# Kernel optimization log

Measured on AMD Instinct MI355X. Metric: run time of the kernel, lower is better.

Reference implementation:

```python
import jax, jax.numpy as jnp
import numpy as np

DIM = 180; HEADS = 6; WS = 16; NUM_TOKENS = 64; RDIM = 10; CAT = 128
KS = 5; MLP_HID = 360; DTD = 64; Hh = 64; Ww = 64; B = 8; M = 64


def _ln(x, g, b, eps=1e-5):
    mu = x.mean(-1, keepdims=True)
    var = ((x - mu) ** 2).mean(-1, keepdims=True)
    return (x - mu) / jnp.sqrt(var + eps) * g + b


def _l2norm(x):
    return x / jnp.clip(jnp.linalg.norm(x, axis=-1, keepdims=True), 1e-12)


def setup_inputs() -> dict:
    key = jax.random.key(0)
    ks = jax.random.split(key, 24)
    rn = lambda k, s: jax.random.normal(k, s, jnp.float32) * 0.02
    z = lambda *s: jnp.zeros(s, jnp.float32)
    return {
        'x': jax.random.normal(ks[0], (B, Hh * Ww, DIM), jnp.float32),
        'td': jax.random.normal(ks[1], (B, M, DIM), jnp.float32),
        'norm1_g': jnp.ones((DIM,), jnp.float32), 'norm1_b': z(DIM),
        'wqkv_w': rn(ks[2], (DIM, 3 * DIM)), 'wqkv_b': z(3 * DIM),
        'atd_wq_w': rn(ks[3], (DIM, RDIM)), 'atd_wq_b': z(RDIM),
        'atd_wk_w': rn(ks[4], (DIM, RDIM)), 'atd_wk_b': z(RDIM),
        'atd_wv_w': rn(ks[5], (DIM, DIM)), 'atd_wv_b': z(DIM),
        'atd_scale': jnp.ones((1,), jnp.float32),
        'aca_proj_w': rn(ks[6], (DIM, DIM)), 'aca_proj_b': z(DIM),
        'win_rpb': rn(ks[7], ((2 * WS - 1) ** 2, HEADS)),
        'win_proj_w': rn(ks[8], (DIM, DIM)), 'win_proj_b': z(DIM),
        'fc_td_w': rn(ks[9], (DIM, DTD)), 'fc_td_b': z(DTD),
        'fc1_w': rn(ks[10], (DIM, MLP_HID)), 'fc1_b': z(MLP_HID),
        'dw_w': rn(ks[11], (MLP_HID + DTD, 1, KS, KS)), 'dw_b': z(MLP_HID + DTD),
        'fc2_w': rn(ks[12], (MLP_HID + DTD, DIM)), 'fc2_b': z(DIM),
        'norm2_g': jnp.ones((DIM,), jnp.float32), 'norm2_b': z(DIM),
        'rpi_sa': jax.random.randint(ks[13], (WS * WS, WS * WS), 0, (2 * WS - 1) ** 2),
        'h': Hh, 'w': Ww,
    }


def reference(x, td, norm1_g, norm1_b, wqkv_w, wqkv_b, atd_wq_w, atd_wq_b,
              atd_wk_w, atd_wk_b, atd_wv_w, atd_wv_b, atd_scale,
              aca_proj_w, aca_proj_b, win_rpb, win_proj_w, win_proj_b,
              fc_td_w, fc_td_b, fc1_w, fc1_b, dw_w, dw_b, fc2_w, fc2_b,
              norm2_g, norm2_b, rpi_sa, h, w):
    b, n, c = x.shape
    hd = c // HEADS
    shortcut = x
    xn = _ln(x, norm1_g, norm1_b)
    qkv = xn @ wqkv_w + wqkv_b  # [b, n, 3c]

    # --- ATD_CA: l2-normalized cross-attention to token dictionary ---
    q = xn @ atd_wq_w + atd_wq_b          # [b, n, rd]
    kk = td @ atd_wk_w + atd_wk_b         # [b, m, rd]
    vv = td @ atd_wv_w + atd_wv_b         # [b, m, c]
    logit_scale = 1.0 + jnp.clip(atd_scale, 0.0, 3.0) * np.log(NUM_TOKENS)
    sim = jnp.einsum('bnr,bmr->bnm', _l2norm(q), _l2norm(kk)) * logit_scale
    attn_atd = jax.nn.softmax(sim, axis=-1)
    x_atd = jnp.einsum('bnm,bmc->bnc', attn_atd, vv)
    tk_id = jnp.argmax(attn_atd, axis=-1)  # [b, n]

    # --- AC_MSA: category-sorted grouped attention ---
    gs = min(n, CAT); ng = (n + gs - 1) // gs; pad_n = ng * gs - n
    sort_idx = jnp.argsort(tk_id, axis=-1)
    inv_idx = jnp.argsort(sort_idx, axis=-1)  # inverse permutation
    sq = jnp.take_along_axis(qkv, sort_idx[:, :, None], axis=1)
    sq = jnp.concatenate([sq, jnp.flip(sq[:, n - pad_n:n, :], axis=1)], axis=1)
    g = sq.reshape(b, ng, gs, 3, HEADS, hd).transpose(3, 0, 1, 4, 2, 5)
    qa, ka, va = g[0], g[1], g[2]          # [b, ng, H, gs, hd]
    a = jax.nn.softmax(jnp.einsum('bgHid,bgHjd->bgHij', qa, ka) * hd ** -0.5, axis=-1)
    y = jnp.einsum('bgHij,bgHjd->bgHid', a, va).transpose(0, 1, 3, 2, 4)
    y = y.reshape(b, n + pad_n, c)[:, :n]
    x_aca = jnp.take_along_axis(y, inv_idx[:, :, None], axis=1) @ aca_proj_w + aca_proj_b

    # --- gather per-token dictionary features for FFN ---
    td_proj = td @ fc_td_w + fc_td_b       # [b, m, dtd]
    x_td = jnp.take_along_axis(td_proj, jnp.broadcast_to(tk_id[:, :, None], (b, n, DTD)), axis=1)

    # --- window attention (shift_size = 0, no mask) ---
    nwh, nww = h // WS, w // WS
    win = qkv.reshape(b, nwh, WS, nww, WS, 3 * c).transpose(0, 1, 3, 2, 4, 5)
    win = win.reshape(-1, WS * WS, 3 * c)
    B_ = win.shape[0]; N = WS * WS
    wq = win.reshape(B_, N, 3, HEADS, hd).transpose(2, 0, 3, 1, 4)
    qw, kw, vw = wq[0] * hd ** -0.5, wq[1], wq[2]
    bias = win_rpb[rpi_sa.reshape(-1)].reshape(N, N, HEADS).transpose(2, 0, 1)[None]
    aw = jax.nn.softmax(jnp.einsum('wHid,wHjd->wHij', qw, kw) + bias, axis=-1)
    ow = jnp.einsum('wHij,wHjd->wHid', aw, vw).transpose(0, 2, 1, 3).reshape(B_, N, c)
    ow = ow @ win_proj_w + win_proj_b
    attn_x = ow.reshape(b, nwh, nww, WS, WS, c).transpose(0, 1, 3, 2, 4, 5).reshape(b, n, c)

    x = shortcut + x_atd + attn_x + x_aca

    # --- ConvFFN_td with depthwise conv branch ---
    x2 = _ln(x, norm2_g, norm2_b)
    h1 = jax.nn.gelu(x2 @ fc1_w + fc1_b, approximate=False)
    hc = jnp.concatenate([h1, x_td], axis=-1)  # [b, n, C]
    C = hc.shape[-1]
    img = jnp.swapaxes(hc, 1, 2).reshape(b, C, h, w)
    conv = jax.lax.conv_general_dilated(img, dw_w, (1, 1), 'SAME',
        dimension_numbers=('NCHW', 'OIHW', 'NCHW'), feature_group_count=C)
    conv = jax.nn.gelu(conv + dw_b[None, :, None, None], approximate=False)
    hc = hc + jnp.swapaxes(conv.reshape(b, C, n), 1, 2)
    return x + hc @ fc2_w + fc2_b
```

## Files before the change

kernel.cpp:

```cpp
#include <hip/hip_runtime.h>
#include <hip/hip_bf16.h>
#include <math.h>

#define BB      8
#define NTOK    4096
#define CDIM    180
#define C3      540
#define NHEADS  6
#define HD      30
#define MDICT   64
#define RD      10
#define DTD     64
#define MHID    360
#define CCAT    424
#define WS      16
#define WIN_N   256
#define GS      128
#define NG      32
#define ROWS    (BB*NTOK)
#define KP1     192
#define KP2     448

typedef __hip_bfloat16 bf16;
typedef short v8s __attribute__((ext_vector_type(8)));
typedef float f32x4 __attribute__((ext_vector_type(4)));
typedef unsigned int u32x4 __attribute__((ext_vector_type(4)));

__device__ __forceinline__ float gelu_exact(float x) {
    return 0.5f * x * (1.0f + erff(x * 0.70710678118654752f));
}
__device__ __forceinline__ float wave_sum(float v) {
    #pragma unroll
    for (int off = 32; off > 0; off >>= 1) v += __shfl_xor(v, off, 64);
    return v;
}
__device__ __forceinline__ unsigned short f2b(float v) {
    unsigned u = __float_as_uint(v);
    return (unsigned short)((u + 0x7FFFu + ((u >> 16) & 1u)) >> 16);
}
__device__ __forceinline__ float b2f(unsigned short h) {
    return __uint_as_float(((unsigned)h) << 16);
}
__device__ __forceinline__ unsigned packbf(float lo, float hi) {
    return (unsigned)f2b(lo) | ((unsigned)f2b(hi) << 16);
}
__device__ __forceinline__ void gload16(const void* g, void* l) {
    __builtin_amdgcn_global_load_lds(
        (const __attribute__((address_space(1))) void*)g,
        (__attribute__((address_space(3))) void*)l, 16, 0, 0);
}

__global__ __launch_bounds__(256) void detect_kernel(const void* __restrict__ x,
                                                     int* __restrict__ flag,
                                                     int* __restrict__ diag)
{
    __shared__ int cnt;
    if (threadIdx.x == 0) { cnt = 0; *diag = 0; }
    __syncthreads();
    const unsigned short* u = (const unsigned short*)x;
    int c = 0;
    for (int i = threadIdx.x; i < 2048; i += 256) {
        unsigned short e = u[2 * i] & 0x7F80;
        if (e >= 0x4300) c++;
    }
    atomicAdd(&cnt, c);
    __syncthreads();
    if (threadIdx.x == 0) *flag = (cnt > 16) ? 1 : 0;
}

#define NCVT 23
struct CvtArgs {
    const void* src[NCVT];
    float* dst[NCVT];
    int cum[NCVT + 1];
};
__global__ __launch_bounds__(256) void convert_all_kernel(CvtArgs a, int total,
        const int* __restrict__ flag)
{
    int i = blockIdx.x * 256 + threadIdx.x;
    if (i >= total) return;
    int s = 0;
    while (i >= a.cum[s + 1]) s++;
    int off = i - a.cum[s];
    if (*flag) a.dst[s][off] = ((const float*)a.src[s])[off];
    else       a.dst[s][off] = __bfloat162float(((const bf16*)a.src[s])[off]);
}

__global__ __launch_bounds__(256) void check_f32_kernel(const float* __restrict__ buf,
        int n, int bit, int* __restrict__ diag)
{
    int i = blockIdx.x * 256 + threadIdx.x;
    if (i >= n) return;
    unsigned u = __float_as_uint(buf[i]);
    if ((u & 0x7F800000u) == 0x7F800000u) atomicOr(diag, bit);
}

__global__ __launch_bounds__(256) void emit_kernel(const float* __restrict__ src,
        void* __restrict__ out, const int* __restrict__ flag,
        const int* __restrict__ diag, int n)
{
    int i = blockIdx.x * 256 + threadIdx.x;
    if (i >= n) return;
    float v = src[i];
    int d = *diag;
    if (d) v = 100.f + 32.f * (float)d;
    if (*flag) ((float*)out)[i] = v;
    else       ((bf16*)out)[i]  = __float2bfloat16(v);
}

__global__ __launch_bounds__(256) void zero_tail_kernel(bf16* __restrict__ buf)
{
    int idx = blockIdx.x * 256 + threadIdx.x;
    int row = idx / 12, c = idx % 12;
    buf[(size_t)row * KP1 + CDIM + c] = __float2bfloat16(0.f);
}

__global__ __launch_bounds__(256) void packW_kernel(const void* __restrict__ W,
        bf16* __restrict__ Wt, int K, int N, int Kpad, int total,
        const int* __restrict__ flag)
{
    int idx = blockIdx.x * 256 + threadIdx.x;
    if (idx >= total) return;
    int n = idx / Kpad, k = idx % Kpad;
    float v = 0.f;
    if (k < K && n < N) {
        size_t src = (size_t)k * N + n;
        v = (*flag) ? ((const float*)W)[src]
                    : __bfloat162float(((const bf16*)W)[src]);
    }
    Wt[idx] = __float2bfloat16(v);
}

__global__ __launch_bounds__(256) void bias_pre_kernel(const int* __restrict__ rpi,
        const float* __restrict__ rpb, float* __restrict__ bias_t)
{
    int idx = blockIdx.x * 256 + threadIdx.x;
    int h = idx >> 16, ij = idx & 65535;
    bias_t[idx] = rpb[rpi[ij] * NHEADS + h];
}

template<bool GELU_, bool ADDRES, bool BIAS_>
__global__ __launch_bounds__(256) void mgemm_kernel(
        const bf16* __restrict__ A, int lda,
        const bf16* __restrict__ Wt, int ldw,
        const float* __restrict__ bias,
        const float* __restrict__ res, int ldr,
        float* __restrict__ outF, int ldo, int N, int K)
{
    __shared__ __align__(16) unsigned short As[128][32];
    __shared__ __align__(16) unsigned short Bs[64][32];
    int tid = threadIdx.x;
    int wave = tid >> 6, lane = tid & 63;
    int quad = lane >> 4, mr = lane & 15;
    int row0 = blockIdx.y * 128, col0 = blockIdx.x * 64;
    int ar = tid >> 2, ac = (tid & 3) * 8;
    f32x4 z = {0.f, 0.f, 0.f, 0.f};
    f32x4 acc[2][4] = {{z, z, z, z}, {z, z, z, z}};
    const unsigned short* Au = (const unsigned short*)A;
    const unsigned short* Wu = (const unsigned short*)Wt;
    for (int k0 = 0; k0 < K; k0 += 32) {
        gload16(&Au[(size_t)(row0 + ar) * lda + k0 + ac],      &As[ar][ac]);
        gload16(&Au[(size_t)(row0 + 64 + ar) * lda + k0 + ac], &As[64 + ar][ac]);
        gload16(&Wu[(size_t)(col0 + ar) * ldw + k0 + ac],      &Bs[ar][ac]);
        __syncthreads();
        v8s bfr[4];
        #pragma unroll
        for (int ni = 0; ni < 4; ni++)
            bfr[ni] = *(const v8s*)&Bs[ni * 16 + mr][quad * 8];
        #pragma unroll
        for (int s = 0; s < 2; s++) {
            v8s a = *(const v8s*)&As[wave * 32 + s * 16 + mr][quad * 8];
            #pragma unroll
            for (int ni = 0; ni < 4; ni++)
                acc[s][ni] = __builtin_amdgcn_mfma_f32_16x16x32_bf16(
                    a, bfr[ni], acc[s][ni], 0, 0, 0);
        }
        __syncthreads();
    }
    #pragma unroll
    for (int ni = 0; ni < 4; ni++) {
        int gc = col0 + ni * 16 + mr;
        if (gc >= N) continue;
        float bv = BIAS_ ? bias[gc] : 0.f;
        #pragma unroll
        for (int s = 0; s < 2; s++) {
            #pragma unroll
            for (int r = 0; r < 4; r++) {
                int gr = row0 + wave * 32 + s * 16 + quad * 4 + r;
                float v = acc[s][ni][r] + bv;
                if (GELU_) v = gelu_exact(v);
                if (ADDRES) v += res[(size_t)gr * ldr + gc];
                outF[(size_t)gr * ldo + gc] = v;
            }
        }
    }
}

__global__ __launch_bounds__(256) void av_mgemm_kernel(
        const bf16* __restrict__ P, const bf16* __restrict__ vvT,
        const float* __restrict__ xres, float* __restrict__ accout)
{
    __shared__ unsigned short As[64][32];
    __shared__ unsigned short Bs[64][32];
    int tid = threadIdx.x;
    int wave = tid >> 6, lane = tid & 63;
    int quad = lane >> 4, mr = lane & 15;
    int row0 = blockIdx.y * 64, col0 = blockIdx.x * 64;
    int bz = blockIdx.z;
    const unsigned short* Au = (const unsigned short*)P + (size_t)bz * NTOK * MDICT;
    const unsigned short* Wu = (const unsigned short*)vvT + (size_t)bz * 192 * MDICT;
    const float* res = xres + (size_t)bz * NTOK * CDIM;
    float* outF = accout + (size_t)bz * NTOK * CDIM;
    f32x4 z = {0.f, 0.f, 0.f, 0.f};
    f32x4 acc[4] = {z, z, z, z};
    for (int k0 = 0; k0 < MDICT; k0 += 32) {
        #pragma unroll
        for (int e = 0; e < 8; e++) {
            int idx = tid * 8 + e;
            int r = idx >> 5, c = idx & 31;
            As[r][c] = Au[(size_t)(row0 + r) * MDICT + k0 + c];
            Bs[r][c] = Wu[(size_t)(col0 + r) * MDICT + k0 + c];
        }
        __syncthreads();
        v8s a;
        #pragma unroll
        for (int j = 0; j < 8; j++) a[j] = (short)As[wave * 16 + mr][quad * 8 + j];
        #pragma unroll
        for (int ni = 0; ni < 4; ni++) {
            v8s b;
            #pragma unroll
            for (int j = 0; j < 8; j++) b[j] = (short)Bs[ni * 16 + mr][quad * 8 + j];
            acc[ni] = __builtin_amdgcn_mfma_f32_16x16x32_bf16(a, b, acc[ni], 0, 0, 0);
        }
        __syncthreads();
    }
    #pragma unroll
    for (int ni = 0; ni < 4; ni++) {
        int gc = col0 + ni * 16 + mr;
        if (gc >= CDIM) continue;
        #pragma unroll
        for (int r = 0; r < 4; r++) {
            int gr = row0 + wave * 16 + quad * 4 + r;
            float v = acc[ni][r] + res[(size_t)gr * CDIM + gc];
            outF[(size_t)gr * CDIM + gc] = v;
        }
    }
}

__global__ __launch_bounds__(256, 4) void win_mfma_kernel(const float* __restrict__ qkv,
        const float* __restrict__ bias_t, bf16* __restrict__ outb)
{
    int b = blockIdx.y;
    int widx = blockIdx.x / NHEADS;
    int hh = blockIdx.x % NHEADS;
    int wy = widx >> 2, wx = widx & 3;
    int tid = threadIdx.x;
    int wave = tid >> 6, lane = tid & 63, quad = lane >> 4, mr = lane & 15;
    __shared__ __align__(16) unsigned short Ks[64][40];
    __shared__ __align__(16) unsigned short Vt[32][80];

    size_t brow = (size_t)b * NTOK;
    const float scq = 0.18257418583505536f;

    v8s aq[4];
    #pragma unroll
    for (int tt = 0; tt < 4; tt++) {
        int m = (wave * 4 + tt) * 16 + mr;
        int nt_ = (wy * WS + (m >> 4)) * 64 + wx * WS + (m & 15);
        const float* qrow = qkv + (brow + nt_) * C3 + hh * HD;
        #pragma unroll
        for (int jj = 0; jj < 8; jj++) {
            int d = quad * 8 + jj;
            float v = (d < HD) ? qrow[d] * scq : 0.f;
            aq[tt][jj] = (short)f2b(v);
        }
    }
    f32x4 z = {0.f, 0.f, 0.f, 0.f};
    f32x4 oacc[4][2] = {{z, z}, {z, z}, {z, z}, {z, z}};
    float m_r[4], l_r[4];
    #pragma unroll
    for (int tt = 0; tt < 4; tt++) { m_r[tt] = -3.0e38f; l_r[tt] = 0.f; }
    const float* btab = bias_t + (size_t)hh * WIN_N * WIN_N;

    for (int kc = 0; kc < WIN_N; kc += 64) {
        {
            int j = tid >> 2, dg = (tid & 3) * 8;
            int tok = kc + j;
            int nt_ = (wy * WS + (tok >> 4)) * 64 + wx * WS + (tok & 15);
            const float* krow = qkv + (brow + nt_) * C3 + CDIM + hh * HD;
            const float* vrow = qkv + (brow + nt_) * C3 + 2 * CDIM + hh * HD;
            v8s kv;
            #pragma unroll
            for (int jj = 0; jj < 8; jj++) {
                int d = dg + jj;
                float kf = (d < HD) ? krow[d] : 0.f;
                float vf = (d < HD) ? vrow[d] : 0.f;
                kv[jj] = (short)f2b(kf);
                Vt[d][j] = f2b(vf);
            }
            *(v8s*)&Ks[j][dg] = kv;
        }
        __syncthreads();
        #pragma unroll
        for (int tt = 0; tt < 4; tt++) {
            f32x4 s[4];
            #pragma unroll
            for (int nt = 0; nt < 4; nt++) {
                v8s bk = *(const v8s*)&Ks[nt * 16 + mr][quad * 8];
                s[nt] = __builtin_amdgcn_mfma_f32_16x16x32_bf16(bk, aq[tt], z, 0, 0, 0);
            }
            int qg = (wave * 4 + tt) * 16 + mr;
            const float* bi = btab + (size_t)qg * WIN_N + kc;
            float mc = -3.0e38f;
            #pragma unroll
            for (int nt = 0; nt < 4; nt++) {
                f32x4 b4 = *(const f32x4*)(bi + nt * 16 + quad * 4);
                s[nt][0] += b4[0]; s[nt][1] += b4[1];
                s[nt][2] += b4[2]; s[nt][3] += b4[3];
                mc = fmaxf(mc, fmaxf(fmaxf(s[nt][0], s[nt][1]),
                                     fmaxf(s[nt][2], s[nt][3])));
            }
            mc = fmaxf(mc, __shfl_xor(mc, 16, 64));
            mc = fmaxf(mc, __shfl_xor(mc, 32, 64));
            float mn = fmaxf(m_r[tt], mc);
            float alpha = __expf(m_r[tt] - mn);
            m_r[tt] = mn;
            float ls = 0.f;
            #pragma unroll
            for (int nt = 0; nt < 4; nt++) {
                #pragma unroll
                for (int r = 0; r < 4; r++) {
                    float pp = __expf(s[nt][r] - mn);
                    ls += pp;
                    s[nt][r] = pp;
                }
            }
            ls += __shfl_xor(ls, 16, 64);
            ls += __shfl_xor(ls, 32, 64);
            l_r[tt] = l_r[tt] * alpha + ls;
            unsigned dpk[4][2];
            #pragma unroll
            for (int nt = 0; nt < 4; nt++) {
                dpk[nt][0] = packbf(s[nt][0], s[nt][1]);
                dpk[nt][1] = packbf(s[nt][2], s[nt][3]);
            }
            #pragma unroll
            for (int r = 0; r < 4; r++) {
                float av = __shfl(alpha, quad * 4 + r, 64);
                oacc[tt][0][r] *= av;
                oacc[tt][1][r] *= av;
            }
            #pragma unroll
            for (int c = 0; c < 2; c++) {
                union { u32x4 u; v8s s8; } afu;
                #pragma unroll
                for (int t = 0; t < 4; t++) {
                    int srcl = (((quad * 2 + (t >> 1)) & 3) << 4) | mr;
                    unsigned r0 = (unsigned)__shfl((int)dpk[2 * c][t & 1], srcl, 64);
                    unsigned r1 = (unsigned)__shfl((int)dpk[2 * c + 1][t & 1], srcl, 64);
                    afu.u[t] = (quad & 2) ? r1 : r0;
                }
                #pragma unroll
                for (int dt = 0; dt < 2; dt++) {
                    v8s bv = *(const v8s*)&Vt[dt * 16 + mr][c * 32 + quad * 8];
                    oacc[tt][dt] = __builtin_amdgcn_mfma_f32_16x16x32_bf16(
                        afu.s8, bv, oacc[tt][dt], 0, 0, 0);
                }
            }
        }
        __syncthreads();
    }
    #pragma unroll
    for (int tt = 0; tt < 4; tt++) {
        float il = 1.f / l_r[tt];
        #pragma unroll
        for (int r = 0; r < 4; r++) {
            float ilr = __shfl(il, quad * 4 + r, 64);
            int m = (wave * 4 + tt) * 16 + quad * 4 + r;
            int nt_ = (wy * WS + (m >> 4)) * 64 + wx * WS + (m & 15);
            #pragma unroll
            for (int dt = 0; dt < 2; dt++) {
                int d = dt * 16 + mr;
                if (d >= HD) continue;
                outb[(brow + nt_) * KP1 + hh * HD + d] =
                    __float2bfloat16(oacc[tt][dt][r] * ilr);
            }
        }
    }
}

__global__ __launch_bounds__(256, 4) void acmsa_mfma_kernel(const float* __restrict__ qkv,
        const int* __restrict__ sidx, bf16* __restrict__ outb)
{
    int b = blockIdx.y;
    int g = blockIdx.x / NHEADS;
    int hh = blockIdx.x % NHEADS;
    int tid = threadIdx.x;
    int wave = tid >> 6, lane = tid & 63, quad = lane >> 4, mr = lane & 15;
    __shared__ int toks[GS];
    __shared__ __align__(16) unsigned short Ks[64][40];
    __shared__ __align__(16) unsigned short Vt[32][80];

    size_t brow = (size_t)b * NTOK;
    if (tid < GS) toks[tid] = sidx[brow + (size_t)g * GS + tid];
    __syncthreads();
    const float scq = 0.18257418583505536f;

    v8s aq[2];
    #pragma unroll
    for (int tt = 0; tt < 2; tt++) {
        int m = (wave * 2 + tt) * 16 + mr;
        const float* qrow = qkv + (brow + toks[m]) * C3 + hh * HD;
        #pragma unroll
        for (int jj = 0; jj < 8; jj++) {
            int d = quad * 8 + jj;
            float v = (d < HD) ? qrow[d] * scq : 0.f;
            aq[tt][jj] = (short)f2b(v);
        }
    }
    f32x4 z = {0.f, 0.f, 0.f, 0.f};
    f32x4 oacc[2][2] = {{z, z}, {z, z}};
    float m_r[2], l_r[2];
    #pragma unroll
    for (int tt = 0; tt < 2; tt++) { m_r[tt] = -3.0e38f; l_r[tt] = 0.f; }

    for (int kc = 0; kc < GS; kc += 64) {
        {
            int j = tid >> 2, dg = (tid & 3) * 8;
            int tok = toks[kc + j];
            const float* krow = qkv + (brow + tok) * C3 + CDIM + hh * HD;
            const float* vrow = qkv + (brow + tok) * C3 + 2 * CDIM + hh * HD;
            v8s kv;
            #pragma unroll
            for (int jj = 0; jj < 8; jj++) {
                int d = dg + jj;
                float kf = (d < HD) ? krow[d] : 0.f;
                float vf = (d < HD) ? vrow[d] : 0.f;
                kv[jj] = (short)f2b(kf);
                Vt[d][j] = f2b(vf);
            }
            *(v8s*)&Ks[j][dg] = kv;
        }
        __syncthreads();
        #pragma unroll
        for (int tt = 0; tt < 2; tt++) {
            f32x4 s[4];
            #pragma unroll
            for (int nt = 0; nt < 4; nt++) {
                v8s bk = *(const v8s*)&Ks[nt * 16 + mr][quad * 8];
                s[nt] = __builtin_amdgcn_mfma_f32_16x16x32_bf16(bk, aq[tt], z, 0, 0, 0);
            }
            float mc = -3.0e38f;
            #pragma unroll
            for (int nt = 0; nt < 4; nt++)
                mc = fmaxf(mc, fmaxf(fmaxf(s[nt][0], s[nt][1]),
                                     fmaxf(s[nt][2], s[nt][3])));
            mc = fmaxf(mc, __shfl_xor(mc, 16, 64));
            mc = fmaxf(mc, __shfl_xor(mc, 32, 64));
            float mn = fmaxf(m_r[tt], mc);
            float alpha = __expf(m_r[tt] - mn);
            m_r[tt] = mn;
            float ls = 0.f;
            #pragma unroll
            for (int nt = 0; nt < 4; nt++) {
                #pragma unroll
                for (int r = 0; r < 4; r++) {
                    float pp = __expf(s[nt][r] - mn);
                    ls += pp;
                    s[nt][r] = pp;
                }
            }
            ls += __shfl_xor(ls, 16, 64);
            ls += __shfl_xor(ls, 32, 64);
            l_r[tt] = l_r[tt] * alpha + ls;
            unsigned dpk[4][2];
            #pragma unroll
            for (int nt = 0; nt < 4; nt++) {
                dpk[nt][0] = packbf(s[nt][0], s[nt][1]);
                dpk[nt][1] = packbf(s[nt][2], s[nt][3]);
            }
            #pragma unroll
            for (int r = 0; r < 4; r++) {
                float av = __shfl(alpha, quad * 4 + r, 64);
                oacc[tt][0][r] *= av;
                oacc[tt][1][r] *= av;
            }
            #pragma unroll
            for (int c = 0; c < 2; c++) {
                union { u32x4 u; v8s s8; } afu;
                #pragma unroll
                for (int t = 0; t < 4; t++) {
                    int srcl = (((quad * 2 + (t >> 1)) & 3) << 4) | mr;
                    unsigned r0 = (unsigned)__shfl((int)dpk[2 * c][t & 1], srcl, 64);
                    unsigned r1 = (unsigned)__shfl((int)dpk[2 * c + 1][t & 1], srcl, 64);
                    afu.u[t] = (quad & 2) ? r1 : r0;
                }
                #pragma unroll
                for (int dt = 0; dt < 2; dt++) {
                    v8s bv = *(const v8s*)&Vt[dt * 16 + mr][c * 32 + quad * 8];
                    oacc[tt][dt] = __builtin_amdgcn_mfma_f32_16x16x32_bf16(
                        afu.s8, bv, oacc[tt][dt], 0, 0, 0);
                }
            }
        }
        __syncthreads();
    }
    #pragma unroll
    for (int tt = 0; tt < 2; tt++) {
        float il = 1.f / l_r[tt];
        #pragma unroll
        for (int r = 0; r < 4; r++) {
            float ilr = __shfl(il, quad * 4 + r, 64);
            int m = (wave * 2 + tt) * 16 + quad * 4 + r;
            int tok = toks[m];
            #pragma unroll
            for (int dt = 0; dt < 2; dt++) {
                int d = dt * 16 + mr;
                if (d >= HD) continue;
                outb[(brow + tok) * KP1 + hh * HD + d] =
                    __float2bfloat16(oacc[tt][dt][r] * ilr);
            }
        }
    }
}

__global__ __launch_bounds__(64) void ln_kernel(const float* __restrict__ x,
        const float* __restrict__ g, const float* __restrict__ be,
        float* __restrict__ out, bf16* __restrict__ outb)
{
    int row = blockIdx.x; int t = threadIdx.x;
    const float* xr = x + (size_t)row * CDIM;
    float v0 = xr[t];
    float v1 = xr[t + 64];
    float v2 = (t < CDIM - 128) ? xr[t + 128] : 0.f;
    float s1 = wave_sum(v0 + v1 + v2);
    float s2 = wave_sum(v0*v0 + v1*v1 + v2*v2);
    float mu = s1 / (float)CDIM;
    float var = s2 / (float)CDIM - mu * mu;
    float rs = rsqrtf(var + 1e-5f);
    float o0 = (v0 - mu) * rs * g[t]      + be[t];
    float o1 = (v1 - mu) * rs * g[t + 64] + be[t + 64];
    float o2 = (t < CDIM - 128) ? ((v2 - mu) * rs * g[t + 128] + be[t + 128]) : 0.f;
    float* o = out + (size_t)row * CDIM;
    o[t] = o0; o[t + 64] = o1;
    if (t < CDIM - 128) o[t + 128] = o2;
    bf16* ob = outb + (size_t)row * KP1;
    ob[t]       = __float2bfloat16(o0);
    ob[t + 64]  = __float2bfloat16(o1);
    ob[t + 128] = __float2bfloat16(o2);
}

__global__ __launch_bounds__(64) void td_pre_kernel(const float* __restrict__ td,
        const float* __restrict__ wk, const float* __restrict__ wkb,
        const float* __restrict__ wv, const float* __restrict__ wvb,
        const float* __restrict__ wtd, const float* __restrict__ wtdb,
        float* __restrict__ kkn, bf16* __restrict__ vvT, float* __restrict__ tdp)
{
    int blk = blockIdx.x;
    int b = blk >> 6, m = blk & 63;
    int t = threadIdx.x;
    __shared__ float tr[CDIM];
    __shared__ float sk[RD];
    __shared__ float snorm;
    const float* tdr = td + (size_t)blk * CDIM;
    tr[t] = tdr[t]; tr[t + 64] = tdr[t + 64];
    if (t < CDIM - 128) tr[t + 128] = tdr[t + 128];
    __syncthreads();
    if (t < RD) {
        float s = wkb[t];
        for (int k = 0; k < CDIM; k++) s += tr[k] * wk[k * RD + t];
        sk[t] = s;
    }
    __syncthreads();
    if (t == 0) {
        float s = 0.f;
        #pragma unroll
        for (int j = 0; j < RD; j++) s += sk[j] * sk[j];
        snorm = fmaxf(sqrtf(s), 1e-12f);
    }
    __syncthreads();
    if (t < RD) kkn[(size_t)blk * RD + t] = sk[t] / snorm;
    for (int c = t; c < 192; c += 64) {
        float s = 0.f;
        if (c < CDIM) {
            s = wvb[c];
            for (int k = 0; k < CDIM; k++) s += tr[k] * wv[k * CDIM + c];
        }
        vvT[((size_t)(b * 192 + c)) * MDICT + m] = __float2bfloat16(s);
    }
    {
        float s = wtdb[t];
        for (int k = 0; k < CDIM; k++) s += tr[k] * wtd[k * DTD + t];
        tdp[(size_t)blk * DTD + t] = s;
    }
}

__global__ __launch_bounds__(64) void atd_soft_kernel(const float* __restrict__ xn,
        const float* __restrict__ wq, const float* __restrict__ wqb,
        const float* __restrict__ scale_p, const float* __restrict__ kkn,
        bf16* __restrict__ Pout, int* __restrict__ tk_id)
{
    int row = blockIdx.x;
    int b = row >> 12;
    int t = threadIdx.x;
    const float* xrow = xn + (size_t)row * CDIM;
    float v0 = xrow[t];
    float v1 = xrow[t + 64];
    float v2 = (t < CDIM - 128) ? xrow[t + 128] : 0.f;
    float sq[RD];
    #pragma unroll
    for (int j = 0; j < RD; j++) {
        float part = v0 * wq[t * RD + j] + v1 * wq[(t + 64) * RD + j];
        if (t < CDIM - 128) part += v2 * wq[(t + 128) * RD + j];
        sq[j] = wave_sum(part) + wqb[j];
    }
    float qn = 0.f;
    #pragma unroll
    for (int j = 0; j < RD; j++) qn += sq[j] * sq[j];
    qn = fmaxf(sqrtf(qn), 1e-12f);
    float ls = 1.0f + fminf(fmaxf(scale_p[0], 0.f), 3.f) * 4.158883083359672f;
    const float* kr = kkn + ((size_t)b * MDICT + t) * RD;
    float s = 0.f;
    #pragma unroll
    for (int j = 0; j < RD; j++) s += sq[j] * kr[j];
    s = s / qn * ls;
    float mv = s; int mi = t;
    #pragma unroll
    for (int off = 32; off > 0; off >>= 1) {
        float ov = __shfl_xor(mv, off, 64);
        int   oi = __shfl_xor(mi, off, 64);
        if (ov > mv || (ov == mv && oi < mi)) { mv = ov; mi = oi; }
    }
    float e = __expf(s - mv);
    float denom = wave_sum(e);
    Pout[(size_t)row * MDICT + t] = __float2bfloat16(e / denom);
    if (t == 0) tk_id[row] = mi;
}

__global__ __launch_bounds__(256) void sort_kernel(const int* __restrict__ tk_id,
                                                   int* __restrict__ sidx)
{
    int b = blockIdx.x; int tid = threadIdx.x;
    __shared__ int keys[NTOK];
    __shared__ int cnt[256];
    __shared__ int off[256];
    const int* kb = tk_id + (size_t)b * NTOK;
    for (int i = tid; i < NTOK; i += 256) keys[i] = kb[i];
    __syncthreads();
    int v = tid >> 2, seg = tid & 3;
    int lo = seg * 1024, hi = lo + 1024;
    int c = 0;
    for (int i = lo; i < hi; i++) c += (keys[i] == v);
    cnt[tid] = c;
    __syncthreads();
    if (tid == 0) {
        int run = 0;
        for (int l = 0; l < 256; l++) { off[l] = run; run += cnt[l]; }
    }
    __syncthreads();
    int o = off[tid];
    int* sb = sidx + (size_t)b * NTOK;
    for (int i = lo; i < hi; i++) if (keys[i] == v) sb[o++] = i;
}

__global__ __launch_bounds__(256) void gather_td_kernel(const int* __restrict__ tk_id,
        const float* __restrict__ tdp, float* __restrict__ hc)
{
    int idx = blockIdx.x * 256 + threadIdx.x;
    int row = idx >> 6, j = idx & 63;
    int b = row >> 12;
    int tk = tk_id[row];
    hc[(size_t)row * CCAT + MHID + j] = tdp[((size_t)b * MDICT + tk) * DTD + j];
}

#define CHK3 64
#define CTW  8
#define CTH  8
#define CHW  12
#define CHP  144
#define CSPX 68
__global__ __launch_bounds__(256) void conv_kernel(const float* __restrict__ hc,
        const float* __restrict__ w, const float* __restrict__ wb,
        bf16* __restrict__ outb)
{
    int ch0 = blockIdx.x * CHK3;
    int tile = blockIdx.y;
    int b = blockIdx.z;
    int ty0 = (tile >> 3) * CTH, tx0 = (tile & 7) * CTW;
    __shared__ __align__(16) float sh[CHP][CSPX];
    __shared__ __align__(16) float wt[25][CHK3];
    int tid = threadIdx.x;
    for (int idx = tid; idx < CHP * CHK3; idx += 256) {
        int pix = idx >> 6, ch = idx & 63;
        int gy = ty0 + pix / CHW - 2, gx = tx0 + pix % CHW - 2;
        int chg = ch0 + ch;
        float v = 0.f;
        if (gy >= 0 && gy < 64 && gx >= 0 && gx < 64 && chg < CCAT)
            v = hc[((size_t)b * NTOK + gy * 64 + gx) * CCAT + chg];
        sh[pix][ch] = v;
    }
    for (int idx = tid; idx < 25 * CHK3; idx += 256) {
        int kk = idx >> 6, ch = idx & 63;
        int chg = ch0 + ch;
        wt[kk][ch] = (chg < CCAT) ? w[chg * 25 + kk] : 0.f;
    }
    __syncthreads();
    int q = tid & 3, p = tid >> 2;
    int px = p & 7, py = p >> 3;
    int cb = q * 16;
    int pc = py * CHW + px;
    v8s pk0, pk1;
    #pragma unroll
    for (int sub = 0; sub < 4; sub++) {
        int cs = cb + sub * 4;
        f32x4 acc = {0.f, 0.f, 0.f, 0.f};
        #pragma unroll
        for (int dy = 0; dy < 5; dy++) {
            #pragma unroll
            for (int dx = 0; dx < 5; dx++) {
                f32x4 sv = *(const f32x4*)&sh[pc + dy * CHW + dx][cs];
                f32x4 wv = *(const f32x4*)&wt[dy * 5 + dx][cs];
                acc += sv * wv;
            }
            __builtin_amdgcn_sched_barrier(0);
        }
        f32x4 ctr = *(const f32x4*)&sh[pc + 2 * CHW + 2][cs];
        #pragma unroll
        for (int c = 0; c < 4; c++) {
            int chg = ch0 + cs + c;
            float v = 0.f;
            if (chg < CCAT) {
                float gv = gelu_exact(acc[c] + wb[chg]);
                v = ctr[c] + gv;
            }
            int lc = sub * 4 + c;
            if (lc < 8) pk0[lc] = (short)f2b(v);
            else        pk1[lc - 8] = (short)f2b(v);
        }
        __builtin_amdgcn_sched_barrier(0);
    }
    size_t obase = ((size_t)b * NTOK + (ty0 + py) * 64 + tx0 + px) * KP2 + ch0 + cb;
    unsigned short* ob = (unsigned short*)outb + obase;
    *(v8s*)ob = pk0;
    *(v8s*)(ob + 8) = pk1;
}

extern "C" void kernel_launch(void* const* d_in, const int* in_sizes, int n_in,
                              void* d_out, int out_size, void* d_ws, size_t ws_size,
                              hipStream_t stream)
{
    (void)n_in; (void)ws_size; (void)out_size;
    const int* rpi = (const int*)d_in[28];

    float* p = (float*)d_ws;
    float* xn    = p; p += (size_t)ROWS * CDIM;
    float* acc   = p; p += (size_t)ROWS * CDIM;
    float* tmp1  = p; p += (size_t)ROWS * CDIM;
    float* qkv   = p; p += (size_t)ROWS * C3;
    float* hcnew = p; p += (size_t)ROWS * CCAT;
    float* kkn   = p; p += (size_t)BB * MDICT * RD;
    bf16*  vvT   = (bf16*)p; p += (size_t)BB * 192 * MDICT / 2;
    float* tdp   = p; p += (size_t)BB * MDICT * DTD;
    int*   tk_id = (int*)p; p += ROWS;
    int*   sidx  = (int*)p; p += ROWS;
    int*   flag  = (int*)p; p += 64;
    int*   diag  = (int*)p; p += 64;
    bf16* wtqkv = (bf16*)p; p += 576 * KP1 / 2;
    bf16* wtaca = (bf16*)p; p += 192 * KP1 / 2;
    bf16* wtwin = (bf16*)p; p += 192 * KP1 / 2;
    bf16* wtfc1 = (bf16*)p; p += 384 * KP1 / 2;
    bf16* wtfc2 = (bf16*)p; p += 192 * KP2 / 2;
    float* cin[28];
    for (int i = 0; i < 28; i++) { cin[i] = p; p += in_sizes[i]; }
    float* bias_t = p; p += (size_t)NHEADS * WIN_N * WIN_N;

    float* hc      = qkv;
    bf16*  xnb     = (bf16*)hcnew;
    bf16*  tmp1b   = (bf16*)(hcnew + (size_t)ROWS * KP1 / 2);
    bf16*  hcnewb2 = (bf16*)hcnew;
    bf16*  Pbuf    = (bf16*)tmp1;

    detect_kernel<<<1, 256, 0, stream>>>(d_in[0], flag, diag);
    {
        CvtArgs ca;
        int total = 0, s = 0;
        for (int i = 0; i < 28; i++) {
            if (i == 4 || i == 13 || i == 16 || i == 20 || i == 24) continue;
            ca.src[s] = d_in[i];
            ca.dst[s] = cin[i];
            ca.cum[s] = total;
            total += in_sizes[i];
            s++;
        }
        ca.cum[s] = total;
        convert_all_kernel<<<(total + 255) / 256, 256, 0, stream>>>(ca, total, flag);
    }
    const float *x = cin[0], *td = cin[1], *n1g = cin[2], *n1b = cin[3],
        *wqkv_b = cin[5], *wq_w = cin[6], *wq_b = cin[7],
        *wk_w = cin[8], *wk_b = cin[9], *wv_w = cin[10], *wv_b = cin[11],
        *atd_scale = cin[12], *aca_b = cin[14], *win_rpb = cin[15],
        *winp_b = cin[17], *fctd_w = cin[18], *fctd_b = cin[19],
        *fc1_b = cin[21], *dw_w = cin[22], *dw_b = cin[23], *fc2_b = cin[25],
        *n2g = cin[26], *n2b = cin[27];

    packW_kernel<<<576 * KP1 / 256, 256, 0, stream>>>(d_in[4],  wtqkv, CDIM, C3,   KP1, 576 * KP1, flag);
    packW_kernel<<<192 * KP1 / 256, 256, 0, stream>>>(d_in[13], wtaca, CDIM, CDIM, KP1, 192 * KP1, flag);
    packW_kernel<<<192 * KP1 / 256, 256, 0, stream>>>(d_in[16], wtwin, CDIM, CDIM, KP1, 192 * KP1, flag);
    packW_kernel<<<384 * KP1 / 256, 256, 0, stream>>>(d_in[20], wtfc1, CDIM, MHID, KP1, 384 * KP1, flag);
    packW_kernel<<<192 * KP2 / 256, 256, 0, stream>>>(d_in[24], wtfc2, CCAT, CDIM, KP2, 192 * KP2, flag);
    bias_pre_kernel<<<NHEADS * WIN_N * WIN_N / 256, 256, 0, stream>>>(rpi, win_rpb, bias_t);

    td_pre_kernel<<<BB * MDICT, 64, 0, stream>>>(td, wk_w, wk_b, wv_w, wv_b,
                                                 fctd_w, fctd_b, kkn, vvT, tdp);
    ln_kernel<<<ROWS, 64, 0, stream>>>(x, n1g, n1b, xn, xnb);
    mgemm_kernel<false, false, true><<<dim3(9, ROWS / 128), 256, 0, stream>>>(
        xnb, KP1, wtqkv, KP1, wqkv_b, nullptr, 0, qkv, C3, C3, KP1);
    atd_soft_kernel<<<ROWS, 64, 0, stream>>>(xn, wq_w, wq_b, atd_scale, kkn, Pbuf, tk_id);
    av_mgemm_kernel<<<dim3(3, NTOK / 64, BB), 256, 0, stream>>>(Pbuf, vvT, x, acc);
    sort_kernel<<<BB, 256, 0, stream>>>(tk_id, sidx);
    zero_tail_kernel<<<ROWS * 12 / 256, 256, 0, stream>>>(tmp1b);
    acmsa_mfma_kernel<<<dim3(NG * NHEADS, BB), 256, 0, stream>>>(qkv, sidx, tmp1b);
    mgemm_kernel<false, true, true><<<dim3(3, ROWS / 128), 256, 0, stream>>>(
        tmp1b, KP1, wtaca, KP1, aca_b, acc, CDIM, acc, CDIM, CDIM, KP1);
    win_mfma_kernel<<<dim3(16 * NHEADS, BB), 256, 0, stream>>>(qkv, bias_t, tmp1b);
    mgemm_kernel<false, true, true><<<dim3(3, ROWS / 128), 256, 0, stream>>>(
        tmp1b, KP1, wtwin, KP1, winp_b, acc, CDIM, acc, CDIM, CDIM, KP1);
    ln_kernel<<<ROWS, 64, 0, stream>>>(acc, n2g, n2b, xn, xnb);
    mgemm_kernel<true, false, true><<<dim3(6, ROWS / 128), 256, 0, stream>>>(
        xnb, KP1, wtfc1, KP1, fc1_b, nullptr, 0, hc, CCAT, MHID, KP1);
    gather_td_kernel<<<ROWS * 64 / 256, 256, 0, stream>>>(tk_id, tdp, hc);
    conv_kernel<<<dim3(7, 64, BB), 256, 0, stream>>>(hc, dw_w, dw_b, hcnewb2);
    mgemm_kernel<false, true, true><<<dim3(3, ROWS / 128), 256, 0, stream>>>(
        hcnewb2, KP2, wtfc2, KP2, fc2_b, acc, CDIM, tmp1, CDIM, CDIM, KP2);
    check_f32_kernel<<<(ROWS * CDIM + 255) / 256, 256, 0, stream>>>(tmp1, ROWS * CDIM, 8, diag);
    emit_kernel<<<(ROWS * CDIM + 255) / 256, 256, 0, stream>>>(
        tmp1, d_out, flag, diag, ROWS * CDIM);
}
```

Baseline: 709.5 us.

## Emit QKV as padded bf16 head layout and pretranspose depthwise conv weights

The QKV GEMM epilogue now writes bf16 into a 576-wide layout with each head padded to 32 dims, with the query scale folded in. The two attention kernels then load Q/K/V with single 16-byte vector reads instead of per-element fp32 loads, bounds checks and conversions. A small kernel zeroes the pad slots. The conv weights are also pretransposed once into a global [25][448] table and read directly, dropping the per-block shared-memory weight staging.

```diff
diff --git a/kernel.cpp b/kernel.cpp
--- a/kernel.cpp
+++ b/kernel.cpp
@@ -20,6 +20,7 @@
 #define ROWS    (BB*NTOK)
 #define KP1     192
 #define KP2     448
+#define QKVP    576
 
 typedef __hip_bfloat16 bf16;
 typedef short v8s __attribute__((ext_vector_type(8)));
@@ -115,6 +116,14 @@
     buf[(size_t)row * KP1 + CDIM + c] = __float2bfloat16(0.f);
 }
 
+__global__ __launch_bounds__(256) void zero_qkvpad_kernel(bf16* __restrict__ qb)
+{
+    int idx = blockIdx.x * 256 + threadIdx.x;
+    int row = idx / 36, r = idx % 36;
+    int sec = r / 12, rr = r % 12, hh = rr >> 1, d = 30 + (rr & 1);
+    qb[(size_t)row * QKVP + sec * 192 + hh * 32 + d] = __float2bfloat16(0.f);
+}
+
 __global__ __launch_bounds__(256) void packW_kernel(const void* __restrict__ W,
         bf16* __restrict__ Wt, int K, int N, int Kpad, int total,
         const int* __restrict__ flag)
@@ -131,6 +140,15 @@
     Wt[idx] = __float2bfloat16(v);
 }
 
+__global__ __launch_bounds__(256) void packWT_kernel(const float* __restrict__ w,
+        float* __restrict__ wT)
+{
+    int idx = blockIdx.x * 256 + threadIdx.x;
+    if (idx >= 25 * KP2) return;
+    int kk = idx / KP2, ch = idx % KP2;
+    wT[idx] = (ch < CCAT) ? w[ch * 25 + kk] : 0.f;
+}
+
 __global__ __launch_bounds__(256) void bias_pre_kernel(const int* __restrict__ rpi,
         const float* __restrict__ rpb, float* __restrict__ bias_t)
 {
@@ -139,7 +157,7 @@
     bias_t[idx] = rpb[rpi[ij] * NHEADS + h];
 }
 
-template<bool GELU_, bool ADDRES, bool BIAS_>
+template<bool GELU_, bool ADDRES, bool BIAS_, int OM>
 __global__ __launch_bounds__(256) void mgemm_kernel(
         const bf16* __restrict__ A, int lda,
         const bf16* __restrict__ Wt, int ldw,
@@ -177,6 +195,29 @@
         }
         __syncthreads();
     }
+    if (OM == 1) {
+        bf16* outb = (bf16*)outF;
+        #pragma unroll
+        for (int ni = 0; ni < 4; ni++) {
+            int gc = col0 + ni * 16 + mr;
+            if (gc >= N) continue;
+            float bv = bias[gc];
+            int sec = gc / 180, rem = gc - sec * 180;
+            int hh = rem / 30, d = rem - hh * 30;
+            int slot = sec * 192 + hh * 32 + d;
+            float sc = (sec == 0) ? 0.18257418583505536f : 1.f;
+            #pragma unroll
+            for (int s = 0; s < 2; s++) {
+                #pragma unroll
+                for (int r = 0; r < 4; r++) {
+                    int gr = row0 + wave * 32 + s * 16 + quad * 4 + r;
+                    outb[(size_t)gr * QKVP + slot] =
+                        __float2bfloat16((acc[s][ni][r] + bv) * sc);
+                }
+            }
+        }
+        return;
+    }
     #pragma unroll
     for (int ni = 0; ni < 4; ni++) {
         int gc = col0 + ni * 16 + mr;
@@ -247,7 +288,7 @@
     }
 }
 
-__global__ __launch_bounds__(256, 4) void win_mfma_kernel(const float* __restrict__ qkv,
+__global__ __launch_bounds__(256, 4) void win_mfma_kernel(const bf16* __restrict__ qkvb,
         const float* __restrict__ bias_t, bf16* __restrict__ outb)
 {
     int b = blockIdx.y;
@@ -260,20 +301,14 @@
     __shared__ __align__(16) unsigned short Vt[32][80];
 
     size_t brow = (size_t)b * NTOK;
-    const float scq = 0.18257418583505536f;
+    const unsigned short* qu = (const unsigned short*)qkvb;
 
     v8s aq[4];
     #pragma unroll
     for (int tt = 0; tt < 4; tt++) {
         int m = (wave * 4 + tt) * 16 + mr;
         int nt_ = (wy * WS + (m >> 4)) * 64 + wx * WS + (m & 15);
-        const float* qrow = qkv + (brow + nt_) * C3 + hh * HD;
-        #pragma unroll
-        for (int jj = 0; jj < 8; jj++) {
-            int d = quad * 8 + jj;
-            float v = (d < HD) ? qrow[d] * scq : 0.f;
-            aq[tt][jj] = (short)f2b(v);
-        }
+        aq[tt] = *(const v8s*)&qu[(brow + nt_) * QKVP + hh * 32 + quad * 8];
     }
     f32x4 z = {0.f, 0.f, 0.f, 0.f};
     f32x4 oacc[4][2] = {{z, z}, {z, z}, {z, z}, {z, z}};
@@ -287,18 +322,13 @@
             int j = tid >> 2, dg = (tid & 3) * 8;
             int tok = kc + j;
             int nt_ = (wy * WS + (tok >> 4)) * 64 + wx * WS + (tok & 15);
-            const float* krow = qkv + (brow + nt_) * C3 + CDIM + hh * HD;
-            const float* vrow = qkv + (brow + nt_) * C3 + 2 * CDIM + hh * HD;
-            v8s kv;
-            #pragma unroll
-            for (int jj = 0; jj < 8; jj++) {
-                int d = dg + jj;
-                float kf = (d < HD) ? krow[d] : 0.f;
-                float vf = (d < HD) ? vrow[d] : 0.f;
-                kv[jj] = (short)f2b(kf);
-                Vt[d][j] = f2b(vf);
-            }
+            const unsigned short* base = qu + (brow + nt_) * QKVP + hh * 32;
+            v8s kv = *(const v8s*)&base[192 + dg];
+            v8s vv = *(const v8s*)&base[384 + dg];
             *(v8s*)&Ks[j][dg] = kv;
+            #pragma unroll
+            for (int jj = 0; jj < 8; jj++)
+                Vt[dg + jj][j] = (unsigned short)vv[jj];
         }
         __syncthreads();
         #pragma unroll
@@ -389,7 +419,7 @@
     }
 }
 
-__global__ __launch_bounds__(256, 4) void acmsa_mfma_kernel(const float* __restrict__ qkv,
+__global__ __launch_bounds__(256, 4) void acmsa_mfma_kernel(const bf16* __restrict__ qkvb,
         const int* __restrict__ sidx, bf16* __restrict__ outb)
 {
     int b = blockIdx.y;
@@ -404,19 +434,13 @@
     size_t brow = (size_t)b * NTOK;
     if (tid < GS) toks[tid] = sidx[brow + (size_t)g * GS + tid];
     __syncthreads();
-    const float scq = 0.18257418583505536f;
+    const unsigned short* qu = (const unsigned short*)qkvb;
 
     v8s aq[2];
     #pragma unroll
     for (int tt = 0; tt < 2; tt++) {
         int m = (wave * 2 + tt) * 16 + mr;
-        const float* qrow = qkv + (brow + toks[m]) * C3 + hh * HD;
-        #pragma unroll
-        for (int jj = 0; jj < 8; jj++) {
-            int d = quad * 8 + jj;
-            float v = (d < HD) ? qrow[d] * scq : 0.f;
-            aq[tt][jj] = (short)f2b(v);
-        }
+        aq[tt] = *(const v8s*)&qu[(brow + toks[m]) * QKVP + hh * 32 + quad * 8];
     }
     f32x4 z = {0.f, 0.f, 0.f, 0.f};
     f32x4 oacc[2][2] = {{z, z}, {z, z}};
@@ -428,18 +452,13 @@
         {
             int j = tid >> 2, dg = (tid & 3) * 8;
             int tok = toks[kc + j];
-            const float* krow = qkv + (brow + tok) * C3 + CDIM + hh * HD;
-            const float* vrow = qkv + (brow + tok) * C3 + 2 * CDIM + hh * HD;
-            v8s kv;
-            #pragma unroll
-            for (int jj = 0; jj < 8; jj++) {
-                int d = dg + jj;
-                float kf = (d < HD) ? krow[d] : 0.f;
-                float vf = (d < HD) ? vrow[d] : 0.f;
-                kv[jj] = (short)f2b(kf);
-                Vt[d][j] = f2b(vf);
-            }
+            const unsigned short* base = qu + (brow + tok) * QKVP + hh * 32;
+            v8s kv = *(const v8s*)&base[192 + dg];
+            v8s vv = *(const v8s*)&base[384 + dg];
             *(v8s*)&Ks[j][dg] = kv;
+            #pragma unroll
+            for (int jj = 0; jj < 8; jj++)
+                Vt[dg + jj][j] = (unsigned short)vv[jj];
         }
         __syncthreads();
         #pragma unroll
@@ -680,7 +699,7 @@
 #define CHP  144
 #define CSPX 68
 __global__ __launch_bounds__(256) void conv_kernel(const float* __restrict__ hc,
-        const float* __restrict__ w, const float* __restrict__ wb,
+        const float* __restrict__ wT, const float* __restrict__ wb,
         bf16* __restrict__ outb)
 {
     int ch0 = blockIdx.x * CHK3;
@@ -688,7 +707,6 @@
     int b = blockIdx.z;
     int ty0 = (tile >> 3) * CTH, tx0 = (tile & 7) * CTW;
     __shared__ __align__(16) float sh[CHP][CSPX];
-    __shared__ __align__(16) float wt[25][CHK3];
     int tid = threadIdx.x;
     for (int idx = tid; idx < CHP * CHK3; idx += 256) {
         int pix = idx >> 6, ch = idx & 63;
@@ -699,11 +717,6 @@
             v = hc[((size_t)b * NTOK + gy * 64 + gx) * CCAT + chg];
         sh[pix][ch] = v;
     }
-    for (int idx = tid; idx < 25 * CHK3; idx += 256) {
-        int kk = idx >> 6, ch = idx & 63;
-        int chg = ch0 + ch;
-        wt[kk][ch] = (chg < CCAT) ? w[chg * 25 + kk] : 0.f;
-    }
     __syncthreads();
     int q = tid & 3, p = tid >> 2;
     int px = p & 7, py = p >> 3;
@@ -713,13 +726,14 @@
     #pragma unroll
     for (int sub = 0; sub < 4; sub++) {
         int cs = cb + sub * 4;
+        const float* wtc = wT + ch0 + cs;
         f32x4 acc = {0.f, 0.f, 0.f, 0.f};
         #pragma unroll
         for (int dy = 0; dy < 5; dy++) {
             #pragma unroll
             for (int dx = 0; dx < 5; dx++) {
                 f32x4 sv = *(const f32x4*)&sh[pc + dy * CHW + dx][cs];
-                f32x4 wv = *(const f32x4*)&wt[dy * 5 + dx][cs];
+                f32x4 wv = *(const f32x4*)&wtc[(dy * 5 + dx) * KP2];
                 acc += sv * wv;
             }
             __builtin_amdgcn_sched_barrier(0);
@@ -773,8 +787,10 @@
     float* cin[28];
     for (int i = 0; i < 28; i++) { cin[i] = p; p += in_sizes[i]; }
     float* bias_t = p; p += (size_t)NHEADS * WIN_N * WIN_N;
+    float* wT     = p; p += 25 * KP2;
 
     float* hc      = qkv;
+    bf16*  qkvb    = (bf16*)qkv;
     bf16*  xnb     = (bf16*)hcnew;
     bf16*  tmp1b   = (bf16*)(hcnew + (size_t)ROWS * KP1 / 2);
     bf16*  hcnewb2 = (bf16*)hcnew;
@@ -809,28 +825,30 @@
     packW_kernel<<<384 * KP1 / 256, 256, 0, stream>>>(d_in[20], wtfc1, CDIM, MHID, KP1, 384 * KP1, flag);
     packW_kernel<<<192 * KP2 / 256, 256, 0, stream>>>(d_in[24], wtfc2, CCAT, CDIM, KP2, 192 * KP2, flag);
     bias_pre_kernel<<<NHEADS * WIN_N * WIN_N / 256, 256, 0, stream>>>(rpi, win_rpb, bias_t);
+    packWT_kernel<<<(25 * KP2 + 255) / 256, 256, 0, stream>>>(dw_w, wT);
 
     td_pre_kernel<<<BB * MDICT, 64, 0, stream>>>(td, wk_w, wk_b, wv_w, wv_b,
                                                  fctd_w, fctd_b, kkn, vvT, tdp);
     ln_kernel<<<ROWS, 64, 0, stream>>>(x, n1g, n1b, xn, xnb);
-    mgemm_kernel<false, false, true><<<dim3(9, ROWS / 128), 256, 0, stream>>>(
-        xnb, KP1, wtqkv, KP1, wqkv_b, nullptr, 0, qkv, C3, C3, KP1);
+    mgemm_kernel<false, false, true, 1><<<dim3(9, ROWS / 128), 256, 0, stream>>>(
+        xnb, KP1, wtqkv, KP1, wqkv_b, nullptr, 0, (float*)qkvb, QKVP, C3, KP1);
+    zero_qkvpad_kernel<<<ROWS * 36 / 256, 256, 0, stream>>>(qkvb);
     atd_soft_kernel<<<ROWS, 64, 0, stream>>>(xn, wq_w, wq_b, atd_scale, kkn, Pbuf, tk_id);
     av_mgemm_kernel<<<dim3(3, NTOK / 64, BB), 256, 0, stream>>>(Pbuf, vvT, x, acc);
     sort_kernel<<<BB, 256, 0, stream>>>(tk_id, sidx);
     zero_tail_kernel<<<ROWS * 12 / 256, 256, 0, stream>>>(tmp1b);
-    acmsa_mfma_kernel<<<dim3(NG * NHEADS, BB), 256, 0, stream>>>(qkv, sidx, tmp1b);
-    mgemm_kernel<false, true, true><<<dim3(3, ROWS / 128), 256, 0, stream>>>(
+    acmsa_mfma_kernel<<<dim3(NG * NHEADS, BB), 256, 0, stream>>>(qkvb, sidx, tmp1b);
+    mgemm_kernel<false, true, true, 0><<<dim3(3, ROWS / 128), 256, 0, stream>>>(
         tmp1b, KP1, wtaca, KP1, aca_b, acc, CDIM, acc, CDIM, CDIM, KP1);
-    win_mfma_kernel<<<dim3(16 * NHEADS, BB), 256, 0, stream>>>(qkv, bias_t, tmp1b);
-    mgemm_kernel<false, true, true><<<dim3(3, ROWS / 128), 256, 0, stream>>>(
+    win_mfma_kernel<<<dim3(16 * NHEADS, BB), 256, 0, stream>>>(qkvb, bias_t, tmp1b);
+    mgemm_kernel<false, true, true, 0><<<dim3(3, ROWS / 128), 256, 0, stream>>>(
         tmp1b, KP1, wtwin, KP1, winp_b, acc, CDIM, acc, CDIM, CDIM, KP1);
     ln_kernel<<<ROWS, 64, 0, stream>>>(acc, n2g, n2b, xn, xnb);
-    mgemm_kernel<true, false, true><<<dim3(6, ROWS / 128), 256, 0, stream>>>(
+    mgemm_kernel<true, false, true, 0><<<dim3(6, ROWS / 128), 256, 0, stream>>>(
         xnb, KP1, wtfc1, KP1, fc1_b, nullptr, 0, hc, CCAT, MHID, KP1);
     gather_td_kernel<<<ROWS * 64 / 256, 256, 0, stream>>>(tk_id, tdp, hc);
-    conv_kernel<<<dim3(7, 64, BB), 256, 0, stream>>>(hc, dw_w, dw_b, hcnewb2);
-    mgemm_kernel<false, true, true><<<dim3(3, ROWS / 128), 256, 0, stream>>>(
+    conv_kernel<<<dim3(7, 64, BB), 256, 0, stream>>>(hc, wT, dw_b, hcnewb2);
+    mgemm_kernel<false, true, true, 0><<<dim3(3, ROWS / 128), 256, 0, stream>>>(
         hcnewb2, KP2, wtfc2, KP2, fc2_b, acc, CDIM, tmp1, CDIM, CDIM, KP2);
     check_f32_kernel<<<(ROWS * CDIM + 255) / 256, 256, 0, stream>>>(tmp1, ROWS * CDIM, 8, diag);
     emit_kernel<<<(ROWS * CDIM + 255) / 256, 256, 0, stream>>>(
```

After: 753.5 us. +6.2%, slower.
